# Kernel tuning notes

Measured on AMD Instinct MI355X. Metric: run time of the kernel, lower is better.

The kernel has to match this reference:

```python
import jax, jax.numpy as jnp
import numpy as np

N_NODES = 20000  # number of batch nodes (static for segment ops)

def setup_inputs() -> dict:
    key = jax.random.key(0)
    N, E, V, D = N_NODES, 640000, 100000, 64
    ks = jax.random.split(key, 8)
    nodes = jax.random.randint(ks[0], (N,), 0, V)
    neigh_idx = jax.random.randint(ks[1], (E,), 0, V)
    seg_ids = jnp.sort(jax.random.randint(ks[2], (E,), 0, N))  # ragged degrees, sorted by node
    u2e = jax.random.normal(ks[3], (V, D), jnp.float32) * 0.02
    s1 = 1.0 / np.sqrt(2 * D)
    s2 = 1.0 / np.sqrt(D)
    att1_w = jax.random.uniform(ks[4], (2 * D, D), jnp.float32, -s1, s1)
    att1_b = jnp.zeros((D,), jnp.float32)
    att2_w = jax.random.uniform(ks[5], (D, D), jnp.float32, -s2, s2)
    att2_b = jnp.zeros((D,), jnp.float32)
    att3_w = jax.random.uniform(ks[6], (D, 1), jnp.float32, -s2, s2)
    att3_b = jnp.zeros((1,), jnp.float32)
    return dict(nodes=nodes, neigh_idx=neigh_idx, seg_ids=seg_ids, u2e=u2e,
                att1_w=att1_w, att1_b=att1_b, att2_w=att2_w, att2_b=att2_b,
                att3_w=att3_w, att3_b=att3_b)


def reference(nodes, neigh_idx, seg_ids, u2e, att1_w, att1_b, att2_w, att2_b, att3_w, att3_b):
    # Ragged per-node neighbor attention, flattened over all edges.
    e_u = u2e[neigh_idx]              # [E, D] neighbor embeddings
    u_rep = u2e[nodes][seg_ids]       # [E, D] center-node embedding broadcast per edge
    x = jnp.concatenate([e_u, u_rep], axis=1)            # [E, 2D]
    x = jax.nn.relu(x @ att1_w + att1_b)                  # [E, D]
    x = jax.nn.relu(x @ att2_w + att2_b)                  # [E, D]
    logits = (x @ att3_w + att3_b)[:, 0]                  # [E]
    # segment softmax over each node's neighbor set
    m = jax.ops.segment_max(logits, seg_ids, num_segments=N_NODES)
    m = jnp.where(jnp.isfinite(m), m, 0.0)                # guard empty segments
    ex = jnp.exp(logits - m[seg_ids])
    denom = jax.ops.segment_sum(ex, seg_ids, num_segments=N_NODES)
    att = ex / jnp.maximum(denom[seg_ids], 1e-9)          # [E]
    # attention-weighted sum of neighbor embeddings per node (e_u^T @ att_w per node)
    out = jax.ops.segment_sum(att[:, None] * e_u, seg_ids, num_segments=N_NODES)  # [N, D]
    return out
```

## Files before the change

kernel.cpp:

```cpp
#include <hip/hip_runtime.h>
#include <hip/hip_bf16.h>

typedef __attribute__((ext_vector_type(8))) short bf16x8;
typedef __attribute__((ext_vector_type(4))) float f32x4;

__device__ __forceinline__ unsigned short f2bf(float f) {
    unsigned x = __float_as_uint(f);
    unsigned r = (x + 0x7FFF + ((x >> 16) & 1)) >> 16;
    return (unsigned short)r;
}
__device__ __forceinline__ bf16x8 cvt8(const float* __restrict__ p) {
    bf16x8 r;
#pragma unroll
    for (int j = 0; j < 8; ++j) r[j] = (short)f2bf(p[j]);
    return r;
}
__device__ __forceinline__ unsigned pack_relu_bf16(unsigned yv, unsigned zv) {
    float lo = fmaxf(__uint_as_float(yv << 16) + __uint_as_float(zv << 16), 0.0f);
    float hi = fmaxf(__uint_as_float(yv & 0xFFFF0000u) + __uint_as_float(zv & 0xFFFF0000u), 0.0f);
    __hip_bfloat162 p = __float22bfloat162_rn(float2{lo, hi});
    return *(unsigned*)&p;
}

template <bool T1>
__launch_bounds__(256)
__global__ void conv_all_k(const float* __restrict__ u2e,
                           const int* __restrict__ nodes,
                           const int* __restrict__ segs,
                           const float* __restrict__ w1,
                           const float* __restrict__ w2,
                           const float* __restrict__ b1f,
                           unsigned short* __restrict__ Y,
                           unsigned short* __restrict__ u2ebf,
                           unsigned short* __restrict__ z,
                           unsigned short* __restrict__ w2t,
                           int* __restrict__ seg_off,
                           float* __restrict__ zout,
                           float* __restrict__ den,
                           int V, int N, int E, int yblk, int zblk,
                           int ytiles, int ztiles) {
    __shared__ __align__(16) unsigned short w1l[64 * 72];
    const int bid = blockIdx.x;
    const int t = threadIdx.x;
    const int wid = t >> 6;
    const int lane = t & 63;
    const int q = lane >> 4;
    const int m15 = lane & 15;

    if (bid < yblk + zblk) {
        const bool isY = bid < yblk;
        const int kbase = isY ? 0 : 64;
        for (int u = t; u < 64 * 16; u += 256) {
            int k = u >> 4;
            int n4 = (u & 15) * 4;
            float4 v = *(const float4*)(w1 + (long)(kbase + k) * 64 + n4);
            w1l[(n4 + 0) * 72 + k] = f2bf(v.x);
            w1l[(n4 + 1) * 72 + k] = f2bf(v.y);
            w1l[(n4 + 2) * 72 + k] = f2bf(v.z);
            w1l[(n4 + 3) * 72 + k] = f2bf(v.w);
        }
        __syncthreads();

        bf16x8 wb0[4], wb1[4];
#pragma unroll
        for (int b = 0; b < 4; ++b) {
            const unsigned short* wr = w1l + (b * 16 + m15) * 72;
            wb0[b] = *(const bf16x8*)(wr + q * 8);
            wb1[b] = *(const bf16x8*)(wr + 32 + q * 8);
        }

        if (isY) {
            for (int tile = bid; tile < ytiles; tile += yblk) {
                const int wbase = tile * 64 + wid * 16;
                if (wbase >= V) continue;
                int row = min(wbase + m15, V - 1);
                const float* p = u2e + (long)row * 64;
                bf16x8 a0 = cvt8(p + q * 8);
                bf16x8 a1 = cvt8(p + 32 + q * 8);
                if (T1 && wbase + m15 < V) {
                    *(bf16x8*)(u2ebf + (long)row * 64 + q * 8) = a0;
                    *(bf16x8*)(u2ebf + (long)row * 64 + 32 + q * 8) = a1;
                }
                f32x4 acc[4];
#pragma unroll
                for (int b = 0; b < 4; ++b) {
                    acc[b] = (f32x4){0.f, 0.f, 0.f, 0.f};
                    acc[b] = __builtin_amdgcn_mfma_f32_16x16x32_bf16(a0, wb0[b], acc[b], 0, 0, 0);
                    acc[b] = __builtin_amdgcn_mfma_f32_16x16x32_bf16(a1, wb1[b], acc[b], 0, 0, 0);
                }
#pragma unroll
                for (int b = 0; b < 4; ++b)
#pragma unroll
                    for (int r = 0; r < 4; ++r) {
                        int rr = wbase + q * 4 + r;
                        if (rr < V) Y[(long)rr * 64 + b * 16 + m15] = f2bf(acc[b][r]);
                    }
            }
        } else {
            float b1v[4];
#pragma unroll
            for (int b = 0; b < 4; ++b) b1v[b] = b1f[b * 16 + m15];
            for (int tile = bid - yblk; tile < ztiles; tile += zblk) {
                const int wbase = tile * 64 + wid * 16;
                if (wbase >= N) continue;
                int nd = nodes[min(wbase + m15, N - 1)];
                const float* p = u2e + (long)nd * 64;
                bf16x8 a0 = cvt8(p + q * 8);
                bf16x8 a1 = cvt8(p + 32 + q * 8);
                f32x4 acc[4];
#pragma unroll
                for (int b = 0; b < 4; ++b) {
                    acc[b] = (f32x4){b1v[b], b1v[b], b1v[b], b1v[b]};
                    acc[b] = __builtin_amdgcn_mfma_f32_16x16x32_bf16(a0, wb0[b], acc[b], 0, 0, 0);
                    acc[b] = __builtin_amdgcn_mfma_f32_16x16x32_bf16(a1, wb1[b], acc[b], 0, 0, 0);
                }
#pragma unroll
                for (int b = 0; b < 4; ++b)
#pragma unroll
                    for (int r = 0; r < 4; ++r) {
                        int rr = wbase + q * 4 + r;
                        if (rr < N) z[(long)rr * 64 + b * 16 + m15] = f2bf(acc[b][r]);
                    }
            }
        }
    } else if (bid == yblk + zblk) {
        for (int i = t; i < 64 * 64; i += 256) {
            int k = i >> 6, n = i & 63;
            w2t[n * 64 + k] = f2bf(w2[i]);
        }
    } else {
        if (T1) {
            long zt = (long)(bid - yblk - zblk - 1) * 256 + t;
            long nth = (long)(gridDim.x - yblk - zblk - 1) * 256;
            f32x4 zz = (f32x4){0.f, 0.f, 0.f, 0.f};
            for (long i = zt; i < (long)N * 16; i += nth) ((f32x4*)zout)[i] = zz;
            for (long i = zt; i < (long)((N + 3) / 4); i += nth) ((f32x4*)den)[i] = zz;
        } else {
            int idx = (bid - yblk - zblk - 1) * 256 + t;
            if (idx > N) return;
            int l = 0, r = E;
            while (l < r) { int mid = (l + r) >> 1; if (segs[mid] < idx) l = mid + 1; else r = mid; }
            seg_off[idx] = l;
        }
    }
}

__launch_bounds__(256)
__global__ void fused_ea_k(const int* __restrict__ neigh,
                           const int* __restrict__ segs,
                           const unsigned short* __restrict__ Y,
                           const unsigned short* __restrict__ z,
                           const unsigned short* __restrict__ u2ebf,
                           const unsigned short* __restrict__ w2t,
                           const float* __restrict__ b2f,
                           const float* __restrict__ w3f,
                           const float* __restrict__ b3f,
                           float* __restrict__ outp,
                           float* __restrict__ den, int E) {
    const int wid = threadIdx.x >> 6;
    const int lane = threadIdx.x & 63;
    const int q = lane >> 4;
    const int m15 = lane & 15;
    const long base = ((long)blockIdx.x * 4 + wid) * 32;
    if (base >= E) return;

    int vi[2], sg[2];
    bool val[2];
#pragma unroll
    for (int g = 0; g < 2; ++g) {
        long e = base + g * 16 + m15;
        val[g] = e < E;
        int ec = (int)(val[g] ? e : (long)E - 1);
        vi[g] = neigh[ec];
        sg[g] = segs[ec];
    }

    unsigned short uv[2][16];
#pragma unroll
    for (int g = 0; g < 2; ++g)
#pragma unroll
        for (int j = 0; j < 16; ++j) {
            int svi = __builtin_amdgcn_readlane(vi[g], j);
            uv[g][j] = u2ebf[((long)svi << 6) + lane];
        }

    bf16x8 y0[2], y1[2], zz0[2], zz1[2];
#pragma unroll
    for (int g = 0; g < 2; ++g) {
        const unsigned short* yr = Y + (long)vi[g] * 64;
        y0[g] = *(const bf16x8*)(yr + q * 8);
        y1[g] = *(const bf16x8*)(yr + 32 + q * 8);
        const unsigned short* zr = z + (long)sg[g] * 64;
        zz0[g] = *(const bf16x8*)(zr + q * 8);
        zz1[g] = *(const bf16x8*)(zr + 32 + q * 8);
    }

    float b2v[4], w3v[4];
#pragma unroll
    for (int b = 0; b < 4; ++b) {
        b2v[b] = b2f[b * 16 + m15];
        w3v[b] = w3f[b * 16 + m15];
    }
    const float b3v = b3f[0];

    f32x4 acc[2][4];
#pragma unroll
    for (int g = 0; g < 2; ++g) {
        bf16x8 h0, h1;
#pragma unroll
        for (int j = 0; j < 4; ++j) {
            ((unsigned*)&h0)[j] = pack_relu_bf16(((unsigned*)&y0[g])[j], ((unsigned*)&zz0[g])[j]);
            ((unsigned*)&h1)[j] = pack_relu_bf16(((unsigned*)&y1[g])[j], ((unsigned*)&zz1[g])[j]);
        }
#pragma unroll
        for (int b = 0; b < 4; ++b) {
            acc[g][b] = (f32x4){b2v[b], b2v[b], b2v[b], b2v[b]};
            const bf16x8* wrow = (const bf16x8*)(w2t + (b * 16 + m15) * 64);
            acc[g][b] = __builtin_amdgcn_mfma_f32_16x16x32_bf16(h0, wrow[0 + q], acc[g][b], 0, 0, 0);
            acc[g][b] = __builtin_amdgcn_mfma_f32_16x16x32_bf16(h1, wrow[4 + q], acc[g][b], 0, 0, 0);
        }
    }

    float exm[2];
#pragma unroll
    for (int g = 0; g < 2; ++g) {
        float ev[4];
#pragma unroll
        for (int r = 0; r < 4; ++r) {
            float v = 0.0f;
#pragma unroll
            for (int b = 0; b < 4; ++b) v += fmaxf(acc[g][b][r], 0.0f) * w3v[b];
            v += __shfl_xor(v, 1);
            v += __shfl_xor(v, 2);
            v += __shfl_xor(v, 4);
            v += __shfl_xor(v, 8);
            ev[r] = __expf(v + b3v);
        }
        int rsel = m15 & 3;
        float exval = rsel == 0 ? ev[0] : (rsel == 1 ? ev[1] : (rsel == 2 ? ev[2] : ev[3]));
        float em = __shfl(exval, ((m15 >> 2) << 4) | (m15 & 3));
        exm[g] = val[g] ? em : 0.0f;
    }

    float a = 0.0f;
    float ds = 0.0f;
    int cur = __builtin_amdgcn_readlane(sg[0], 0);
#pragma unroll
    for (int g = 0; g < 2; ++g)
#pragma unroll
        for (int j = 0; j < 16; ++j) {
            int ssg = __builtin_amdgcn_readlane(sg[g], j);
            float sex = __uint_as_float(
                (unsigned)__builtin_amdgcn_readlane(__float_as_uint(exm[g]), j));
            if (ssg != cur) {
                atomicAdd(outp + (long)cur * 64 + lane, a);
                if (lane == 0) atomicAdd(den + cur, ds);
                a = 0.0f; ds = 0.0f; cur = ssg;
            }
            a = fmaf(sex, __uint_as_float((unsigned)uv[g][j] << 16), a);
            ds += sex;
        }
    atomicAdd(outp + (long)cur * 64 + lane, a);
    if (lane == 0) atomicAdd(den + cur, ds);
}

__launch_bounds__(256)
__global__ void div_k(float* __restrict__ out, const float* __restrict__ den, int N) {
    int i = blockIdx.x * 256 + threadIdx.x;
    if (i >= N * 16) return;
    float inv = 1.0f / fmaxf(den[i >> 4], 1e-9f);
    f32x4* p = (f32x4*)out + i;
    f32x4 v = *p;
    v[0] *= inv; v[1] *= inv; v[2] *= inv; v[3] *= inv;
    *p = v;
}

__launch_bounds__(256)
__global__ void logits2_k(const int* __restrict__ neigh,
                          const int* __restrict__ segs,
                          const unsigned short* __restrict__ Y,
                          const unsigned short* __restrict__ z,
                          const unsigned short* __restrict__ w2t,
                          const float* __restrict__ b2f,
                          const float* __restrict__ w3f, const float* __restrict__ b3f,
                          float* __restrict__ ex, int E) {
    const int wid = threadIdx.x >> 6;
    const int lane = threadIdx.x & 63;
    const int q = lane >> 4;
    const int m15 = lane & 15;
    const long base = ((long)blockIdx.x * 4 + wid) * 32;
    if (base >= E) return;

    int vi[2], sg[2];
#pragma unroll
    for (int g = 0; g < 2; ++g) {
        long e = base + g * 16 + m15;
        int ec = (int)(e < E ? e : (long)E - 1);
        vi[g] = neigh[ec];
        sg[g] = segs[ec];
    }
    bf16x8 y0[2], y1[2], zz0[2], zz1[2];
#pragma unroll
    for (int g = 0; g < 2; ++g) {
        const unsigned short* yr = Y + (long)vi[g] * 64;
        y0[g] = *(const bf16x8*)(yr + q * 8);
        y1[g] = *(const bf16x8*)(yr + 32 + q * 8);
        const unsigned short* zr = z + (long)sg[g] * 64;
        zz0[g] = *(const bf16x8*)(zr + q * 8);
        zz1[g] = *(const bf16x8*)(zr + 32 + q * 8);
    }

    float b2v[4], w3v[4];
#pragma unroll
    for (int b = 0; b < 4; ++b) {
        b2v[b] = b2f[b * 16 + m15];
        w3v[b] = w3f[b * 16 + m15];
    }

    f32x4 acc[2][4];
#pragma unroll
    for (int g = 0; g < 2; ++g) {
        bf16x8 h0, h1;
#pragma unroll
        for (int j = 0; j < 4; ++j) {
            ((unsigned*)&h0)[j] = pack_relu_bf16(((unsigned*)&y0[g])[j], ((unsigned*)&zz0[g])[j]);
            ((unsigned*)&h1)[j] = pack_relu_bf16(((unsigned*)&y1[g])[j], ((unsigned*)&zz1[g])[j]);
        }
#pragma unroll
        for (int b = 0; b < 4; ++b) {
            acc[g][b] = (f32x4){b2v[b], b2v[b], b2v[b], b2v[b]};
            const bf16x8* wrow = (const bf16x8*)(w2t + (b * 16 + m15) * 64);
            acc[g][b] = __builtin_amdgcn_mfma_f32_16x16x32_bf16(h0, wrow[0 + q], acc[g][b], 0, 0, 0);
            acc[g][b] = __builtin_amdgcn_mfma_f32_16x16x32_bf16(h1, wrow[4 + q], acc[g][b], 0, 0, 0);
        }
    }

    const float b3v = b3f[0];
#pragma unroll
    for (int g = 0; g < 2; ++g)
#pragma unroll
        for (int r = 0; r < 4; ++r) {
            float v = 0.0f;
#pragma unroll
            for (int b = 0; b < 4; ++b) v += fmaxf(acc[g][b][r], 0.0f) * w3v[b];
            v += __shfl_xor(v, 1);
            v += __shfl_xor(v, 2);
            v += __shfl_xor(v, 4);
            v += __shfl_xor(v, 8);
            long ee = base + g * 16 + q * 4 + r;
            if (m15 == r && ee < E) ex[ee] = __expf(v + b3v);
        }
}

__launch_bounds__(256)
__global__ void aggw_f32_k(const int* __restrict__ seg_off,
                           const int* __restrict__ neigh,
                           const float* __restrict__ u2e,
                           const float* __restrict__ ex,
                           float* __restrict__ out, int N) {
    const int wid = threadIdx.x >> 6;
    const int lane = threadIdx.x & 63;
    const int n = blockIdx.x * 4 + wid;
    if (n >= N) return;
    const int lo = seg_off[n];
    const int hi = seg_off[n + 1];
    const int slot = lane >> 3;
    const int cl = lane & 7;

    float a[8] = {0.f, 0.f, 0.f, 0.f, 0.f, 0.f, 0.f, 0.f};
    float s = 0.0f;

    for (int e = lo + slot; e < hi; e += 8) {
        float w = ex[e];
        int vi = neigh[e];
        s += w;
        const float* row = u2e + (long)vi * 64 + cl * 8;
        float4 v0 = *(const float4*)row;
        float4 v1 = *(const float4*)(row + 4);
        a[0] = fmaf(w, v0.x, a[0]); a[1] = fmaf(w, v0.y, a[1]);
        a[2] = fmaf(w, v0.z, a[2]); a[3] = fmaf(w, v0.w, a[3]);
        a[4] = fmaf(w, v1.x, a[4]); a[5] = fmaf(w, v1.y, a[5]);
        a[6] = fmaf(w, v1.z, a[6]); a[7] = fmaf(w, v1.w, a[7]);
    }
#pragma unroll
    for (int msk = 8; msk <= 32; msk <<= 1) {
        s += __shfl_xor(s, msk);
#pragma unroll
        for (int j = 0; j < 8; ++j) a[j] += __shfl_xor(a[j], msk);
    }
    if (slot == 0) {
        float inv = 1.0f / fmaxf(s, 1e-9f);
        float4 o0 = {a[0] * inv, a[1] * inv, a[2] * inv, a[3] * inv};
        float4 o1 = {a[4] * inv, a[5] * inv, a[6] * inv, a[7] * inv};
        float* op = out + (long)n * 64 + cl * 8;
        *(float4*)op = o0;
        *(float4*)(op + 4) = o1;
    }
}

__global__ void prep_bounds_k(const float* __restrict__ w1,
                              const float* __restrict__ w2,
                              const int* __restrict__ segs,
                              unsigned short* __restrict__ w1t,
                              unsigned short* __restrict__ w2t,
                              int* __restrict__ seg_off, int N, int E) {
    int t = threadIdx.x;
    if (blockIdx.x == 0) {
        for (int i = t; i < 128 * 64; i += 256) {
            int k = i >> 6, n = i & 63;
            w1t[n * 128 + k] = f2bf(w1[i]);
        }
        for (int i = t; i < 64 * 64; i += 256) {
            int k = i >> 6, n = i & 63;
            w2t[n * 64 + k] = f2bf(w2[i]);
        }
    } else {
        int idx = (blockIdx.x - 1) * 256 + t;
        if (idx > N) return;
        int l = 0, r = E;
        while (l < r) { int mid = (l + r) >> 1; if (segs[mid] < idx) l = mid + 1; else r = mid; }
        seg_off[idx] = l;
    }
}

__launch_bounds__(256)
__global__ void logits_fb_k(const int* __restrict__ nodes,
                            const int* __restrict__ neigh,
                            const int* __restrict__ segs,
                            const float* __restrict__ u2e,
                            const unsigned short* __restrict__ w1t,
                            const unsigned short* __restrict__ w2t,
                            const float* __restrict__ b1f, const float* __restrict__ b2f,
                            const float* __restrict__ w3f, const float* __restrict__ b3f,
                            float* __restrict__ ex, int E) {
    __shared__ __align__(16) unsigned short h1buf[4][16 * 72];
    const int wid = threadIdx.x >> 6;
    const int lane = threadIdx.x & 63;
    const int q = lane >> 4;
    const int m15 = lane & 15;
    const long base = ((long)blockIdx.x * 4 + wid) * 16;
    long ee0 = base + m15;
    int e = (int)(ee0 < E ? ee0 : (long)E - 1);
    int ni = neigh[e];
    int ctr = nodes[segs[e]];
    const float* eu = u2e + (long)ni * 64;
    const float* ur = u2e + (long)ctr * 64;
    bf16x8 a0 = cvt8(eu + q * 8), a1 = cvt8(eu + 32 + q * 8);
    bf16x8 a2 = cvt8(ur + q * 8), a3 = cvt8(ur + 32 + q * 8);
    f32x4 acc[4];
#pragma unroll
    for (int b = 0; b < 4; ++b) {
        float bvv = b1f[b * 16 + m15];
        acc[b] = (f32x4){bvv, bvv, bvv, bvv};
        const bf16x8* wrow = (const bf16x8*)(w1t + (b * 16 + m15) * 128);
        acc[b] = __builtin_amdgcn_mfma_f32_16x16x32_bf16(a0, wrow[0 + q], acc[b], 0, 0, 0);
        acc[b] = __builtin_amdgcn_mfma_f32_16x16x32_bf16(a1, wrow[4 + q], acc[b], 0, 0, 0);
        acc[b] = __builtin_amdgcn_mfma_f32_16x16x32_bf16(a2, wrow[8 + q], acc[b], 0, 0, 0);
        acc[b] = __builtin_amdgcn_mfma_f32_16x16x32_bf16(a3, wrow[12 + q], acc[b], 0, 0, 0);
    }
#pragma unroll
    for (int b = 0; b < 4; ++b)
#pragma unroll
        for (int r = 0; r < 4; ++r)
            h1buf[wid][(q * 4 + r) * 72 + b * 16 + m15] = f2bf(fmaxf(acc[b][r], 0.0f));
    const unsigned short* hrow = &h1buf[wid][m15 * 72];
    bf16x8 h0 = *(const bf16x8*)(hrow + q * 8);
    bf16x8 h1 = *(const bf16x8*)(hrow + 32 + q * 8);
    f32x4 acc2[4];
#pragma unroll
    for (int b = 0; b < 4; ++b) {
        float bvv = b2f[b * 16 + m15];
        acc2[b] = (f32x4){bvv, bvv, bvv, bvv};
        const bf16x8* wrow = (const bf16x8*)(w2t + (b * 16 + m15) * 64);
        acc2[b] = __builtin_amdgcn_mfma_f32_16x16x32_bf16(h0, wrow[0 + q], acc2[b], 0, 0, 0);
        acc2[b] = __builtin_amdgcn_mfma_f32_16x16x32_bf16(h1, wrow[4 + q], acc2[b], 0, 0, 0);
    }
    float b3v = b3f[0];
#pragma unroll
    for (int r = 0; r < 4; ++r) {
        float v = 0.0f;
#pragma unroll
        for (int b = 0; b < 4; ++b) v += fmaxf(acc2[b][r], 0.0f) * w3f[b * 16 + m15];
        v += __shfl_xor(v, 1);
        v += __shfl_xor(v, 2);
        v += __shfl_xor(v, 4);
        v += __shfl_xor(v, 8);
        long ee = base + q * 4 + r;
        if (m15 == r && ee < E) ex[ee] = __expf(v + b3v);
    }
}

extern "C" void kernel_launch(void* const* d_in, const int* in_sizes, int n_in,
                              void* d_out, int out_size, void* d_ws, size_t ws_size,
                              hipStream_t stream) {
    const int* nodes = (const int*)d_in[0];
    const int* neigh = (const int*)d_in[1];
    const int* segs  = (const int*)d_in[2];
    const float* u2e = (const float*)d_in[3];
    const float* w1  = (const float*)d_in[4];
    const float* b1  = (const float*)d_in[5];
    const float* w2  = (const float*)d_in[6];
    const float* b2  = (const float*)d_in[7];
    const float* w3  = (const float*)d_in[8];
    const float* b3  = (const float*)d_in[9];
    const int N = in_sizes[0];
    const int E = in_sizes[1];
    const long VD = in_sizes[3];
    const int V = (int)(VD / 64);

    char* ws = (char*)d_ws;
    size_t off = 0;
    auto alloc = [&](size_t bytes) { char* p = ws + off; off = (off + bytes + 255) & ~(size_t)255; return p; };
    float* ex = (float*)alloc((size_t)E * 4);
    int* seg_off = (int*)alloc((size_t)(N + 1) * 4);
    unsigned short* w1t = (unsigned short*)alloc(128 * 64 * 2);
    unsigned short* w2t = (unsigned short*)alloc(64 * 64 * 2);
    size_t need_min = off;
    unsigned short* Y = (unsigned short*)alloc((size_t)VD * 2);
    unsigned short* zb = (unsigned short*)alloc((size_t)N * 64 * 2);
    size_t need_t2 = off;
    unsigned short* u2ebf = (unsigned short*)alloc((size_t)VD * 2);
    float* den = (float*)alloc((size_t)N * 4);
    size_t need_t1 = off;
    (void)need_min;

    float* out = (float*)d_out;

    const int ytiles = (V + 63) / 64;
    const int ztiles = (N + 63) / 64;
    const int yblk = ytiles < 640 ? ytiles : 640;
    const int zblk = ztiles < 160 ? ztiles : 160;
    const int bblocks = (N + 256) / 256;
    const int lblocks = ((E + 31) / 32 + 3) / 4;
    const int ablocks = (N + 3) / 4;
    const int ZBLK = 128;

    if (ws_size >= need_t1) {
        conv_all_k<true><<<yblk + zblk + 1 + ZBLK, 256, 0, stream>>>(
            u2e, nodes, segs, w1, w2, b1, Y, u2ebf, zb, w2t, nullptr, out, den,
            V, N, E, yblk, zblk, ytiles, ztiles);
        fused_ea_k<<<lblocks, 256, 0, stream>>>(
            neigh, segs, Y, zb, u2ebf, w2t, b2, w3, b3, out, den, E);
        div_k<<<(N * 16 + 255) / 256, 256, 0, stream>>>(out, den, N);
    } else if (ws_size >= need_t2) {
        conv_all_k<false><<<yblk + zblk + 1 + bblocks, 256, 0, stream>>>(
            u2e, nodes, segs, w1, w2, b1, Y, nullptr, zb, w2t, seg_off, nullptr, nullptr,
            V, N, E, yblk, zblk, ytiles, ztiles);
        logits2_k<<<lblocks, 256, 0, stream>>>(neigh, segs, Y, zb, w2t, b2, w3, b3, ex, E);
        aggw_f32_k<<<ablocks, 256, 0, stream>>>(seg_off, neigh, u2e, ex, out, N);
    } else {
        const int pbblocks = 1 + (N + 256) / 256;
        prep_bounds_k<<<pbblocks, 256, 0, stream>>>(w1, w2, segs, w1t, w2t, seg_off, N, E);
        const int blocks1 = ((E + 15) / 16 + 3) / 4;
        logits_fb_k<<<blocks1, 256, 0, stream>>>(nodes, neigh, segs, u2e, w1t, w2t,
                                                 b1, b2, w3, b3, ex, E);
        aggw_f32_k<<<ablocks, 256, 0, stream>>>(seg_off, neigh, u2e, ex, out, N);
    }
}
```

Before: 147.4 us.

## Split weight prep into separate kernel and use one tile per block in conversion

The fused conversion kernel is split in two. A small prep kernel transposes W1/W2 to bf16 and zeroes the output and denominator. A conversion kernel then launches one block per 64-row tile and reads the pre-transposed W1 straight from global memory, instead of every persistent block rebuilding it in shared memory. The fp32 row loads in cvt8 also become two float4 loads. This removes the per-block LDS transpose and barrier and raises parallelism, at the cost of one extra kernel launch and a serial dependency on the prep kernel.

New measurement: 160.0 us. 8.5% more time.

```diff
diff --git a/kernel.cpp b/kernel.cpp
--- a/kernel.cpp
+++ b/kernel.cpp
@@ -10,9 +10,13 @@
     return (unsigned short)r;
 }
 __device__ __forceinline__ bf16x8 cvt8(const float* __restrict__ p) {
+    float4 v0 = *(const float4*)p;
+    float4 v1 = *(const float4*)(p + 4);
     bf16x8 r;
-#pragma unroll
-    for (int j = 0; j < 8; ++j) r[j] = (short)f2bf(p[j]);
+    r[0] = (short)f2bf(v0.x); r[1] = (short)f2bf(v0.y);
+    r[2] = (short)f2bf(v0.z); r[3] = (short)f2bf(v0.w);
+    r[4] = (short)f2bf(v1.x); r[5] = (short)f2bf(v1.y);
+    r[6] = (short)f2bf(v1.z); r[7] = (short)f2bf(v1.w);
     return r;
 }
 __device__ __forceinline__ unsigned pack_relu_bf16(unsigned yv, unsigned zv) {
@@ -22,126 +26,106 @@
     return *(unsigned*)&p;
 }
 
-template <bool T1>
-__launch_bounds__(256)
-__global__ void conv_all_k(const float* __restrict__ u2e,
-                           const int* __restrict__ nodes,
-                           const int* __restrict__ segs,
-                           const float* __restrict__ w1,
-                           const float* __restrict__ w2,
-                           const float* __restrict__ b1f,
-                           unsigned short* __restrict__ Y,
-                           unsigned short* __restrict__ u2ebf,
-                           unsigned short* __restrict__ z,
-                           unsigned short* __restrict__ w2t,
-                           int* __restrict__ seg_off,
-                           float* __restrict__ zout,
-                           float* __restrict__ den,
-                           int V, int N, int E, int yblk, int zblk,
-                           int ytiles, int ztiles) {
-    __shared__ __align__(16) unsigned short w1l[64 * 72];
+__launch_bounds__(256)
+__global__ void prep_t1_k(const float* __restrict__ w1,
+                          const float* __restrict__ w2,
+                          unsigned short* __restrict__ w1t,
+                          unsigned short* __restrict__ w2t,
+                          float* __restrict__ zout,
+                          float* __restrict__ den, int N) {
     const int bid = blockIdx.x;
     const int t = threadIdx.x;
-    const int wid = t >> 6;
-    const int lane = t & 63;
-    const int q = lane >> 4;
-    const int m15 = lane & 15;
-
-    if (bid < yblk + zblk) {
-        const bool isY = bid < yblk;
-        const int kbase = isY ? 0 : 64;
-        for (int u = t; u < 64 * 16; u += 256) {
-            int k = u >> 4;
-            int n4 = (u & 15) * 4;
-            float4 v = *(const float4*)(w1 + (long)(kbase + k) * 64 + n4);
-            w1l[(n4 + 0) * 72 + k] = f2bf(v.x);
-            w1l[(n4 + 1) * 72 + k] = f2bf(v.y);
-            w1l[(n4 + 2) * 72 + k] = f2bf(v.z);
-            w1l[(n4 + 3) * 72 + k] = f2bf(v.w);
-        }
-        __syncthreads();
-
-        bf16x8 wb0[4], wb1[4];
-#pragma unroll
-        for (int b = 0; b < 4; ++b) {
-            const unsigned short* wr = w1l + (b * 16 + m15) * 72;
-            wb0[b] = *(const bf16x8*)(wr + q * 8);
-            wb1[b] = *(const bf16x8*)(wr + 32 + q * 8);
-        }
-
-        if (isY) {
-            for (int tile = bid; tile < ytiles; tile += yblk) {
-                const int wbase = tile * 64 + wid * 16;
-                if (wbase >= V) continue;
-                int row = min(wbase + m15, V - 1);
-                const float* p = u2e + (long)row * 64;
-                bf16x8 a0 = cvt8(p + q * 8);
-                bf16x8 a1 = cvt8(p + 32 + q * 8);
-                if (T1 && wbase + m15 < V) {
-                    *(bf16x8*)(u2ebf + (long)row * 64 + q * 8) = a0;
-                    *(bf16x8*)(u2ebf + (long)row * 64 + 32 + q * 8) = a1;
-                }
-                f32x4 acc[4];
-#pragma unroll
-                for (int b = 0; b < 4; ++b) {
-                    acc[b] = (f32x4){0.f, 0.f, 0.f, 0.f};
-                    acc[b] = __builtin_amdgcn_mfma_f32_16x16x32_bf16(a0, wb0[b], acc[b], 0, 0, 0);
-                    acc[b] = __builtin_amdgcn_mfma_f32_16x16x32_bf16(a1, wb1[b], acc[b], 0, 0, 0);
-                }
-#pragma unroll
-                for (int b = 0; b < 4; ++b)
-#pragma unroll
-                    for (int r = 0; r < 4; ++r) {
-                        int rr = wbase + q * 4 + r;
-                        if (rr < V) Y[(long)rr * 64 + b * 16 + m15] = f2bf(acc[b][r]);
-                    }
-            }
-        } else {
-            float b1v[4];
-#pragma unroll
-            for (int b = 0; b < 4; ++b) b1v[b] = b1f[b * 16 + m15];
-            for (int tile = bid - yblk; tile < ztiles; tile += zblk) {
-                const int wbase = tile * 64 + wid * 16;
-                if (wbase >= N) continue;
-                int nd = nodes[min(wbase + m15, N - 1)];
-                const float* p = u2e + (long)nd * 64;
-                bf16x8 a0 = cvt8(p + q * 8);
-                bf16x8 a1 = cvt8(p + 32 + q * 8);
-                f32x4 acc[4];
-#pragma unroll
-                for (int b = 0; b < 4; ++b) {
-                    acc[b] = (f32x4){b1v[b], b1v[b], b1v[b], b1v[b]};
-                    acc[b] = __builtin_amdgcn_mfma_f32_16x16x32_bf16(a0, wb0[b], acc[b], 0, 0, 0);
-                    acc[b] = __builtin_amdgcn_mfma_f32_16x16x32_bf16(a1, wb1[b], acc[b], 0, 0, 0);
-                }
-#pragma unroll
-                for (int b = 0; b < 4; ++b)
-#pragma unroll
-                    for (int r = 0; r < 4; ++r) {
-                        int rr = wbase + q * 4 + r;
-                        if (rr < N) z[(long)rr * 64 + b * 16 + m15] = f2bf(acc[b][r]);
-                    }
-            }
-        }
-    } else if (bid == yblk + zblk) {
+    if (bid == 0) {
+        for (int i = t; i < 128 * 64; i += 256) {
+            int k = i >> 6, n = i & 63;
+            w1t[n * 128 + k] = f2bf(w1[i]);
+        }
+    } else if (bid == 1) {
         for (int i = t; i < 64 * 64; i += 256) {
             int k = i >> 6, n = i & 63;
             w2t[n * 64 + k] = f2bf(w2[i]);
         }
     } else {
-        if (T1) {
-            long zt = (long)(bid - yblk - zblk - 1) * 256 + t;
-            long nth = (long)(gridDim.x - yblk - zblk - 1) * 256;
-            f32x4 zz = (f32x4){0.f, 0.f, 0.f, 0.f};
-            for (long i = zt; i < (long)N * 16; i += nth) ((f32x4*)zout)[i] = zz;
-            for (long i = zt; i < (long)((N + 3) / 4); i += nth) ((f32x4*)den)[i] = zz;
-        } else {
-            int idx = (bid - yblk - zblk - 1) * 256 + t;
-            if (idx > N) return;
-            int l = 0, r = E;
-            while (l < r) { int mid = (l + r) >> 1; if (segs[mid] < idx) l = mid + 1; else r = mid; }
-            seg_off[idx] = l;
-        }
+        long zt = (long)(bid - 2) * 256 + t;
+        long nth = (long)(gridDim.x - 2) * 256;
+        f32x4 zz = (f32x4){0.f, 0.f, 0.f, 0.f};
+        for (long i = zt; i < (long)N * 16; i += nth) ((f32x4*)zout)[i] = zz;
+        for (long i = zt; i < (long)((N + 3) / 4); i += nth) ((f32x4*)den)[i] = zz;
+    }
+}
+
+__launch_bounds__(256)
+__global__ void conv_t1_k(const float* __restrict__ u2e,
+                          const int* __restrict__ nodes,
+                          const unsigned short* __restrict__ w1t,
+                          const float* __restrict__ b1f,
+                          unsigned short* __restrict__ u2ebf,
+                          unsigned short* __restrict__ Y,
+                          unsigned short* __restrict__ z,
+                          int V, int N, int ytiles) {
+    const int bid = blockIdx.x;
+    const int wid = (threadIdx.x >> 6);
+    const int lane = threadIdx.x & 63;
+    const int q = lane >> 4;
+    const int m15 = lane & 15;
+    const bool isY = bid < ytiles;
+    const int kbase = isY ? 0 : 64;
+
+    bf16x8 wb0[4], wb1[4];
+#pragma unroll
+    for (int b = 0; b < 4; ++b) {
+        const unsigned short* wr = w1t + (b * 16 + m15) * 128 + kbase;
+        wb0[b] = *(const bf16x8*)(wr + q * 8);
+        wb1[b] = *(const bf16x8*)(wr + 32 + q * 8);
+    }
+
+    if (isY) {
+        const int wbase = bid * 64 + wid * 16;
+        if (wbase >= V) return;
+        int row = min(wbase + m15, V - 1);
+        const float* p = u2e + (long)row * 64;
+        bf16x8 a0 = cvt8(p + q * 8);
+        bf16x8 a1 = cvt8(p + 32 + q * 8);
+        if (wbase + m15 < V) {
+            *(bf16x8*)(u2ebf + (long)row * 64 + q * 8) = a0;
+            *(bf16x8*)(u2ebf + (long)row * 64 + 32 + q * 8) = a1;
+        }
+        f32x4 acc[4];
+#pragma unroll
+        for (int b = 0; b < 4; ++b) {
+            acc[b] = (f32x4){0.f, 0.f, 0.f, 0.f};
+            acc[b] = __builtin_amdgcn_mfma_f32_16x16x32_bf16(a0, wb0[b], acc[b], 0, 0, 0);
+            acc[b] = __builtin_amdgcn_mfma_f32_16x16x32_bf16(a1, wb1[b], acc[b], 0, 0, 0);
+        }
+#pragma unroll
+        for (int b = 0; b < 4; ++b)
+#pragma unroll
+            for (int r = 0; r < 4; ++r) {
+                int rr = wbase + q * 4 + r;
+                if (rr < V) Y[(long)rr * 64 + b * 16 + m15] = f2bf(acc[b][r]);
+            }
+    } else {
+        const int wbase = (bid - ytiles) * 64 + wid * 16;
+        if (wbase >= N) return;
+        int nd = nodes[min(wbase + m15, N - 1)];
+        const float* p = u2e + (long)nd * 64;
+        bf16x8 a0 = cvt8(p + q * 8);
+        bf16x8 a1 = cvt8(p + 32 + q * 8);
+        f32x4 acc[4];
+#pragma unroll
+        for (int b = 0; b < 4; ++b) {
+            float bv = b1f[b * 16 + m15];
+            acc[b] = (f32x4){bv, bv, bv, bv};
+            acc[b] = __builtin_amdgcn_mfma_f32_16x16x32_bf16(a0, wb0[b], acc[b], 0, 0, 0);
+            acc[b] = __builtin_amdgcn_mfma_f32_16x16x32_bf16(a1, wb1[b], acc[b], 0, 0, 0);
+        }
+#pragma unroll
+        for (int b = 0; b < 4; ++b)
+#pragma unroll
+            for (int r = 0; r < 4; ++r) {
+                int rr = wbase + q * 4 + r;
+                if (rr < N) z[(long)rr * 64 + b * 16 + m15] = f2bf(acc[b][r]);
+            }
     }
 }
 
@@ -273,6 +257,113 @@
     f32x4 v = *p;
     v[0] *= inv; v[1] *= inv; v[2] *= inv; v[3] *= inv;
     *p = v;
+}
+
+__launch_bounds__(256)
+__global__ void conv_t2_k(const float* __restrict__ u2e,
+                          const int* __restrict__ nodes,
+                          const int* __restrict__ segs,
+                          const float* __restrict__ w1,
+                          const float* __restrict__ w2,
+                          const float* __restrict__ b1f,
+                          unsigned short* __restrict__ Y,
+                          unsigned short* __restrict__ z,
+                          unsigned short* __restrict__ w2t,
+                          int* __restrict__ seg_off,
+                          int V, int N, int E, int yblk, int zblk,
+                          int ytiles, int ztiles) {
+    __shared__ __align__(16) unsigned short w1l[64 * 72];
+    const int bid = blockIdx.x;
+    const int t = threadIdx.x;
+    const int wid = t >> 6;
+    const int lane = t & 63;
+    const int q = lane >> 4;
+    const int m15 = lane & 15;
+
+    if (bid < yblk + zblk) {
+        const bool isY = bid < yblk;
+        const int kbase = isY ? 0 : 64;
+        for (int u = t; u < 64 * 16; u += 256) {
+            int k = u >> 4;
+            int n4 = (u & 15) * 4;
+            float4 v = *(const float4*)(w1 + (long)(kbase + k) * 64 + n4);
+            w1l[(n4 + 0) * 72 + k] = f2bf(v.x);
+            w1l[(n4 + 1) * 72 + k] = f2bf(v.y);
+            w1l[(n4 + 2) * 72 + k] = f2bf(v.z);
+            w1l[(n4 + 3) * 72 + k] = f2bf(v.w);
+        }
+        __syncthreads();
+
+        bf16x8 wb0[4], wb1[4];
+#pragma unroll
+        for (int b = 0; b < 4; ++b) {
+            const unsigned short* wr = w1l + (b * 16 + m15) * 72;
+            wb0[b] = *(const bf16x8*)(wr + q * 8);
+            wb1[b] = *(const bf16x8*)(wr + 32 + q * 8);
+        }
+
+        if (isY) {
+            for (int tile = bid; tile < ytiles; tile += yblk) {
+                const int wbase = tile * 64 + wid * 16;
+                if (wbase >= V) continue;
+                int row = min(wbase + m15, V - 1);
+                const float* p = u2e + (long)row * 64;
+                bf16x8 a0 = cvt8(p + q * 8);
+                bf16x8 a1 = cvt8(p + 32 + q * 8);
+                f32x4 acc[4];
+#pragma unroll
+                for (int b = 0; b < 4; ++b) {
+                    acc[b] = (f32x4){0.f, 0.f, 0.f, 0.f};
+                    acc[b] = __builtin_amdgcn_mfma_f32_16x16x32_bf16(a0, wb0[b], acc[b], 0, 0, 0);
+                    acc[b] = __builtin_amdgcn_mfma_f32_16x16x32_bf16(a1, wb1[b], acc[b], 0, 0, 0);
+                }
+#pragma unroll
+                for (int b = 0; b < 4; ++b)
+#pragma unroll
+                    for (int r = 0; r < 4; ++r) {
+                        int rr = wbase + q * 4 + r;
+                        if (rr < V) Y[(long)rr * 64 + b * 16 + m15] = f2bf(acc[b][r]);
+                    }
+            }
+        } else {
+            float b1v[4];
+#pragma unroll
+            for (int b = 0; b < 4; ++b) b1v[b] = b1f[b * 16 + m15];
+            for (int tile = bid - yblk; tile < ztiles; tile += zblk) {
+                const int wbase = tile * 64 + wid * 16;
+                if (wbase >= N) continue;
+                int nd = nodes[min(wbase + m15, N - 1)];
+                const float* p = u2e + (long)nd * 64;
+                bf16x8 a0 = cvt8(p + q * 8);
+                bf16x8 a1 = cvt8(p + 32 + q * 8);
+                f32x4 acc[4];
+#pragma unroll
+                for (int b = 0; b < 4; ++b) {
+                    acc[b] = (f32x4){b1v[b], b1v[b], b1v[b], b1v[b]};
+                    acc[b] = __builtin_amdgcn_mfma_f32_16x16x32_bf16(a0, wb0[b], acc[b], 0, 0, 0);
+                    acc[b] = __builtin_amdgcn_mfma_f32_16x16x32_bf16(a1, wb1[b], acc[b], 0, 0, 0);
+                }
+#pragma unroll
+                for (int b = 0; b < 4; ++b)
+#pragma unroll
+                    for (int r = 0; r < 4; ++r) {
+                        int rr = wbase + q * 4 + r;
+                        if (rr < N) z[(long)rr * 64 + b * 16 + m15] = f2bf(acc[b][r]);
+                    }
+            }
+        }
+    } else if (bid == yblk + zblk) {
+        for (int i = t; i < 64 * 64; i += 256) {
+            int k = i >> 6, n = i & 63;
+            w2t[n * 64 + k] = f2bf(w2[i]);
+        }
+    } else {
+        int idx = (bid - yblk - zblk - 1) * 256 + t;
+        if (idx > N) return;
+        int l = 0, r = E;
+        while (l < r) { int mid = (l + r) >> 1; if (segs[mid] < idx) l = mid + 1; else r = mid; }
+        seg_off[idx] = l;
+    }
 }
 
 __launch_bounds__(256)
@@ -533,18 +624,17 @@
     const int bblocks = (N + 256) / 256;
     const int lblocks = ((E + 31) / 32 + 3) / 4;
     const int ablocks = (N + 3) / 4;
-    const int ZBLK = 128;
 
     if (ws_size >= need_t1) {
-        conv_all_k<true><<<yblk + zblk + 1 + ZBLK, 256, 0, stream>>>(
-            u2e, nodes, segs, w1, w2, b1, Y, u2ebf, zb, w2t, nullptr, out, den,
-            V, N, E, yblk, zblk, ytiles, ztiles);
+        prep_t1_k<<<128, 256, 0, stream>>>(w1, w2, w1t, w2t, out, den, N);
+        conv_t1_k<<<ytiles + ztiles, 256, 0, stream>>>(
+            u2e, nodes, w1t, b1, u2ebf, Y, zb, V, N, ytiles);
         fused_ea_k<<<lblocks, 256, 0, stream>>>(
             neigh, segs, Y, zb, u2ebf, w2t, b2, w3, b3, out, den, E);
         div_k<<<(N * 16 + 255) / 256, 256, 0, stream>>>(out, den, N);
     } else if (ws_size >= need_t2) {
-        conv_all_k<false><<<yblk + zblk + 1 + bblocks, 256, 0, stream>>>(
-            u2e, nodes, segs, w1, w2, b1, Y, nullptr, zb, w2t, seg_off, nullptr, nullptr,
+        conv_t2_k<<<yblk + zblk + 1 + bblocks, 256, 0, stream>>>(
+            u2e, nodes, segs, w1, w2, b1, Y, zb, w2t, seg_off,
             V, N, E, yblk, zblk, ytiles, ztiles);
         logits2_k<<<lblocks, 256, 0, stream>>>(neigh, segs, Y, zb, w2t, b2, w3, b3, ex, E);
         aggw_f32_k<<<ablocks, 256, 0, stream>>>(seg_off, neigh, u2e, ex, out, N);
```
